# Kernel tuning notes

Measured on AMD Instinct MI355X. Metric: run time of the kernel, lower is better.

## Reference

```python
import jax, jax.numpy as jnp
import numpy as np

B, C, K, T = 8, 256, 64, 1000
NORM_EPS = 1e-12


def setup_inputs() -> dict:
    key = jax.random.key(0)
    k_x, k_codes, k_scales = jax.random.split(key, 3)
    init_val = 1.0 / (K * C) ** 0.5
    x = jax.random.normal(k_x, (B, C, T), dtype=jnp.float32)
    codes = jax.random.uniform(k_codes, (C, K), dtype=jnp.float32,
                               minval=-init_val, maxval=init_val)
    scales = jax.random.uniform(k_scales, (K,), dtype=jnp.float32,
                                minval=0.0, maxval=1.0)
    return {"x": x, "codes": codes, "scales": scales}


def l2_normalize(t, axis, eps=NORM_EPS):
    n = jnp.sqrt(jnp.sum(t * t, axis=axis, keepdims=True))
    n = jnp.maximum(n, eps)
    return t / n


def reference(x, codes, scales):
    # x: (B, C, T); codes: (C, K); scales: (K,)
    residual = x[:, :, None, :] - codes[None, :, :, None]      # (B, C, K, T)
    residual_l2sqr = jnp.sum(residual * residual, axis=1)      # (B, K, T)
    weights_tc = jax.nn.softmax(-scales[None, :, None] * residual_l2sqr, axis=1)  # softmax over codes K
    embeddings = jnp.einsum('bckt,bkt->bkc', residual, weights_tc) / x.shape[-1]  # (B, K, C)
    embeddings = l2_normalize(embeddings, axis=-1)
    return embeddings
```

## Files before the change

kernel.cpp:

```cpp
#include <hip/hip_runtime.h>
#include <stdint.h>

constexpr int Bn  = 8;
constexpr int Cn  = 256;
constexpr int Kn  = 64;
constexpr int Tn  = 1000;
constexpr int CH  = 16;
constexpr int NCH = 64;

constexpr int XT_P = 264;
constexpr int MW_P = 20;

typedef float f32x4 __attribute__((ext_vector_type(4)));
typedef __bf16 bf16x8 __attribute__((ext_vector_type(8)));

__device__ __forceinline__ unsigned short f2bf(float f) {
    unsigned u = __float_as_uint(f);
    return (unsigned short)((u + 0x7FFFu + ((u >> 16) & 1u)) >> 16);
}

union BF8 { unsigned short u[8]; bf16x8 v; };

__global__ __launch_bounds__(256) void lde_w(
    const float* __restrict__ x,
    const float* __restrict__ codes,
    const float* __restrict__ scales,
    unsigned short* __restrict__ w_g,
    float* __restrict__ Sp)
{
    __shared__ __align__(16) unsigned short xT[CH * XT_P];
    __shared__ float Mw[Kn * MW_P];
    __shared__ float xsqp[64 * 17];
    __shared__ float xsq4[64];
    __shared__ float csqs[Kn];
    __shared__ float spw[4 * 64];

    const int tid  = threadIdx.x;
    const int wave = tid >> 6;
    const int lane = tid & 63;
    const int n    = lane & 15;
    const int q    = lane >> 4;
    const int b    = blockIdx.x >> 6;
    const int ch   = blockIdx.x & 63;
    const int t0   = ch * CH;
    const float* xb = x + (size_t)b * Cn * Tn;

    {
        const int tf = tid & 3;
        float sq0 = 0.f, sq1 = 0.f, sq2 = 0.f, sq3 = 0.f;
#pragma unroll
        for (int r = 0; r < 4; ++r) {
            int c = (tid >> 2) + 64 * r;
            int t = t0 + 4 * tf;
            float4 v;
            if (t + 3 < Tn) {
                v = *(const float4*)(xb + c * Tn + t);
            } else {
                v.x = (t     < Tn) ? xb[c * Tn + t]     : 0.f;
                v.y = (t + 1 < Tn) ? xb[c * Tn + t + 1] : 0.f;
                v.z = (t + 2 < Tn) ? xb[c * Tn + t + 2] : 0.f;
                v.w = (t + 3 < Tn) ? xb[c * Tn + t + 3] : 0.f;
            }
            xT[(4 * tf + 0) * XT_P + c] = f2bf(v.x);
            xT[(4 * tf + 1) * XT_P + c] = f2bf(v.y);
            xT[(4 * tf + 2) * XT_P + c] = f2bf(v.z);
            xT[(4 * tf + 3) * XT_P + c] = f2bf(v.w);
            sq0 = fmaf(v.x, v.x, sq0);
            sq1 = fmaf(v.y, v.y, sq1);
            sq2 = fmaf(v.z, v.z, sq2);
            sq3 = fmaf(v.w, v.w, sq3);
        }
        float* xp = xsqp + (tid >> 2) * 17 + 4 * tf;
        xp[0] = sq0; xp[1] = sq1; xp[2] = sq2; xp[3] = sq3;
    }
    __syncthreads();

    if (lane < 16) {
        float a = 0.f;
#pragma unroll
        for (int i = 0; i < 16; ++i) a += xsqp[(wave * 16 + i) * 17 + lane];
        xsq4[wave * 16 + lane] = a;
    }

    {
        const int kglob = wave * 16 + n;
        const float* cod = codes + (q * 8) * Kn + kglob;
        float csq_part = 0.f;
        f32x4 acc = {0.f, 0.f, 0.f, 0.f};
#pragma unroll
        for (int c0 = 0; c0 < Cn; c0 += 32) {
            float cf[8];
#pragma unroll
            for (int j = 0; j < 8; ++j) cf[j] = cod[(size_t)(c0 + j) * Kn];
            BF8 aF;
#pragma unroll
            for (int j = 0; j < 8; ++j) {
                csq_part = fmaf(cf[j], cf[j], csq_part);
                aF.u[j] = f2bf(cf[j]);
            }
            bf16x8 bF = *(const bf16x8*)(xT + n * XT_P + c0 + q * 8);
            acc = __builtin_amdgcn_mfma_f32_16x16x32_bf16(aF.v, bF, acc, 0, 0, 0);
        }
        csq_part += __shfl_xor(csq_part, 16, 64);
        csq_part += __shfl_xor(csq_part, 32, 64);
        if (q == 0) csqs[kglob] = csq_part;
#pragma unroll
        for (int r = 0; r < 4; ++r)
            Mw[(wave * 16 + q * 4 + r) * MW_P + n] = acc[r];
    }
    __syncthreads();

    {
        const float sc = scales[lane];
        const float cq = csqs[lane];
        unsigned short wh[4];
        float sp = 0.f;
#pragma unroll
        for (int j = 0; j < 4; ++j) {
            int t = wave * 4 + j;
            float xs_t  = xsq4[t] + xsq4[16 + t] + xsq4[32 + t] + xsq4[48 + t];
            float m     = Mw[lane * MW_P + t];
            float logit = -sc * (xs_t - 2.f * m + cq);
            float mx = logit;
#pragma unroll
            for (int off = 32; off >= 1; off >>= 1)
                mx = fmaxf(mx, __shfl_xor(mx, off, 64));
            float e = __expf(logit - mx);
            float s = e;
#pragma unroll
            for (int off = 32; off >= 1; off >>= 1)
                s += __shfl_xor(s, off, 64);
            float wv = e / s;
            if (t0 + t >= Tn) wv = 0.f;
            sp += wv;
            wh[j] = f2bf(wv);
        }
        *(ushort4*)(w_g + ((size_t)(b * NCH + ch) * Kn + lane) * CH + wave * 4) =
            make_ushort4(wh[0], wh[1], wh[2], wh[3]);
        spw[wave * 64 + lane] = sp;
    }
    __syncthreads();
    if (wave == 0) {
        float s4 = spw[lane] + spw[64 + lane] + spw[128 + lane] + spw[192 + lane];
        Sp[((size_t)b * Kn + lane) * NCH + ch] = s4;
    }
}

__global__ __launch_bounds__(64) void lde_gemm(
    const float* __restrict__ x,
    const unsigned short* __restrict__ w_g,
    float* __restrict__ Ew)
{
    const int lane = threadIdx.x;
    const int n    = lane & 15;
    const int q    = lane >> 4;
    const int bid  = blockIdx.x;
    const int kt   = bid & 3;
    const int ct   = (bid >> 2) & 15;
    const int b    = bid >> 6;

    const float* xrow = x + (size_t)(b * Cn + ct * 16 + n) * Tn;
    const unsigned short* wbase =
        w_g + (size_t)b * NCH * Kn * CH + (kt * 16 + n) * CH + (q & 1) * 8;
    const int qh = q >> 1;

    f32x4 acc = {0.f, 0.f, 0.f, 0.f};
#pragma unroll 4
    for (int tc = 0; tc < 31; ++tc) {
        bf16x8 aF = *(const bf16x8*)(wbase + (size_t)(2 * tc + qh) * (Kn * CH));
        float4 v0 = *(const float4*)(xrow + tc * 32 + q * 8);
        float4 v1 = *(const float4*)(xrow + tc * 32 + q * 8 + 4);
        BF8 bF;
        bF.u[0] = f2bf(v0.x); bF.u[1] = f2bf(v0.y);
        bF.u[2] = f2bf(v0.z); bF.u[3] = f2bf(v0.w);
        bF.u[4] = f2bf(v1.x); bF.u[5] = f2bf(v1.y);
        bF.u[6] = f2bf(v1.z); bF.u[7] = f2bf(v1.w);
        acc = __builtin_amdgcn_mfma_f32_16x16x32_bf16(aF, bF.v, acc, 0, 0, 0);
    }
    {
        bf16x8 aF = *(const bf16x8*)(wbase + (size_t)(62 + qh) * (Kn * CH));
        const int tbase = 31 * 32 + q * 8;
        BF8 bF;
#pragma unroll
        for (int j = 0; j < 8; ++j) {
            int t = tbase + j;
            bF.u[j] = (t < Tn) ? f2bf(xrow[t]) : (unsigned short)0;
        }
        acc = __builtin_amdgcn_mfma_f32_16x16x32_bf16(aF, bF.v, acc, 0, 0, 0);
    }
    float* er = Ew + ((size_t)b * Kn + kt * 16 + q * 4) * Cn + ct * 16 + n;
#pragma unroll
    for (int r = 0; r < 4; ++r)
        er[(size_t)r * Cn] = acc[r];
}

__global__ __launch_bounds__(256) void lde_fin(
    const float* __restrict__ Ew,
    const float* __restrict__ Sp,
    const float* __restrict__ codes,
    float* __restrict__ out)
{
    const int b    = blockIdx.x >> 6;
    const int k    = blockIdx.x & 63;
    const int tid  = threadIdx.x;
    const int lane = tid & 63;
    const int wave = tid >> 6;

    __shared__ float red[4];
    __shared__ float Ss;

    if (wave == 0) {
        float s = Sp[((size_t)b * Kn + k) * NCH + lane];
#pragma unroll
        for (int off = 32; off >= 1; off >>= 1) s += __shfl_xor(s, off, 64);
        if (lane == 0) Ss = s;
    }
    __syncthreads();
    const float S = Ss;

    const int c = tid;
    float val = Ew[((size_t)b * Kn + k) * Cn + c];
    float e = (val - codes[c * Kn + k] * S) * (1.0f / (float)Tn);

    float qq = e * e;
#pragma unroll
    for (int off = 32; off >= 1; off >>= 1) qq += __shfl_xor(qq, off, 64);
    if (lane == 0) red[wave] = qq;
    __syncthreads();
    float nn = sqrtf(red[0] + red[1] + red[2] + red[3]);

    out[((size_t)b * Kn + k) * Cn + c] = e / fmaxf(nn, 1e-12f);
}

extern "C" void kernel_launch(void* const* d_in, const int* in_sizes, int n_in,
                              void* d_out, int out_size, void* d_ws, size_t ws_size,
                              hipStream_t stream) {
    const float* x      = (const float*)d_in[0];
    const float* codes  = (const float*)d_in[1];
    const float* scales = (const float*)d_in[2];
    float* out = (float*)d_out;

    char* ws = (char*)d_ws;
    unsigned short* w_g = (unsigned short*)ws;
    float*          Sp  = (float*)(ws + (1u << 20));
    float*          Ew  = (float*)(ws + (1u << 20) + (128u << 10));

    lde_w   <<<Bn * NCH,     256, 0, stream>>>(x, codes, scales, w_g, Sp);
    lde_gemm<<<Bn * 16 * 4,  64,  0, stream>>>(x, w_g, Ew);
    lde_fin <<<Bn * Kn,      256, 0, stream>>>(Ew, Sp, codes, out);
}
```

Baseline: 76.12 us.

## Fuse GEMM and finalize kernels, stage x as padded bf16 in workspace

The first kernel now also writes a bf16 copy of x, padded to 1024 columns with zero fill, into workspace. The separate GEMM and normalize kernels are merged into one 512-thread kernel per (batch, k-tile). Each wave computes two c-tiles from the bf16 x copy, then applies the code-weight correction and the L2 normalization in-block. This removes a kernel launch, the Ew intermediate round-trip and the per-iteration fp32-to-bf16 conversion. The cost is that the fused kernel launches only 32 blocks, which leaves most CUs idle and puts the long 32-step reduction on a few waves.

```diff
diff --git a/kernel.cpp b/kernel.cpp
--- a/kernel.cpp
+++ b/kernel.cpp
@@ -5,6 +5,7 @@
 constexpr int Cn  = 256;
 constexpr int Kn  = 64;
 constexpr int Tn  = 1000;
+constexpr int TP  = 1024;
 constexpr int CH  = 16;
 constexpr int NCH = 64;
 
@@ -25,6 +26,7 @@
     const float* __restrict__ x,
     const float* __restrict__ codes,
     const float* __restrict__ scales,
+    unsigned short* __restrict__ xbf,
     unsigned short* __restrict__ w_g,
     float* __restrict__ Sp)
 {
@@ -61,10 +63,12 @@
                 v.z = (t + 2 < Tn) ? xb[c * Tn + t + 2] : 0.f;
                 v.w = (t + 3 < Tn) ? xb[c * Tn + t + 3] : 0.f;
             }
-            xT[(4 * tf + 0) * XT_P + c] = f2bf(v.x);
-            xT[(4 * tf + 1) * XT_P + c] = f2bf(v.y);
-            xT[(4 * tf + 2) * XT_P + c] = f2bf(v.z);
-            xT[(4 * tf + 3) * XT_P + c] = f2bf(v.w);
+            ushort4 h = make_ushort4(f2bf(v.x), f2bf(v.y), f2bf(v.z), f2bf(v.w));
+            xT[(4 * tf + 0) * XT_P + c] = h.x;
+            xT[(4 * tf + 1) * XT_P + c] = h.y;
+            xT[(4 * tf + 2) * XT_P + c] = h.z;
+            xT[(4 * tf + 3) * XT_P + c] = h.w;
+            *(ushort4*)(xbf + (((size_t)(b * Cn + c)) << 10) + t0 + 4 * tf) = h;
             sq0 = fmaf(v.x, v.x, sq0);
             sq1 = fmaf(v.y, v.y, sq1);
             sq2 = fmaf(v.z, v.z, sq2);
@@ -146,90 +150,90 @@
     }
 }
 
-__global__ __launch_bounds__(64) void lde_gemm(
-    const float* __restrict__ x,
+__global__ __launch_bounds__(512) void lde_pf(
+    const unsigned short* __restrict__ xbf,
     const unsigned short* __restrict__ w_g,
-    float* __restrict__ Ew)
-{
-    const int lane = threadIdx.x;
-    const int n    = lane & 15;
-    const int q    = lane >> 4;
-    const int bid  = blockIdx.x;
-    const int kt   = bid & 3;
-    const int ct   = (bid >> 2) & 15;
-    const int b    = bid >> 6;
-
-    const float* xrow = x + (size_t)(b * Cn + ct * 16 + n) * Tn;
-    const unsigned short* wbase =
-        w_g + (size_t)b * NCH * Kn * CH + (kt * 16 + n) * CH + (q & 1) * 8;
-    const int qh = q >> 1;
-
-    f32x4 acc = {0.f, 0.f, 0.f, 0.f};
-#pragma unroll 4
-    for (int tc = 0; tc < 31; ++tc) {
-        bf16x8 aF = *(const bf16x8*)(wbase + (size_t)(2 * tc + qh) * (Kn * CH));
-        float4 v0 = *(const float4*)(xrow + tc * 32 + q * 8);
-        float4 v1 = *(const float4*)(xrow + tc * 32 + q * 8 + 4);
-        BF8 bF;
-        bF.u[0] = f2bf(v0.x); bF.u[1] = f2bf(v0.y);
-        bF.u[2] = f2bf(v0.z); bF.u[3] = f2bf(v0.w);
-        bF.u[4] = f2bf(v1.x); bF.u[5] = f2bf(v1.y);
-        bF.u[6] = f2bf(v1.z); bF.u[7] = f2bf(v1.w);
-        acc = __builtin_amdgcn_mfma_f32_16x16x32_bf16(aF, bF.v, acc, 0, 0, 0);
-    }
-    {
-        bf16x8 aF = *(const bf16x8*)(wbase + (size_t)(62 + qh) * (Kn * CH));
-        const int tbase = 31 * 32 + q * 8;
-        BF8 bF;
-#pragma unroll
-        for (int j = 0; j < 8; ++j) {
-            int t = tbase + j;
-            bF.u[j] = (t < Tn) ? f2bf(xrow[t]) : (unsigned short)0;
-        }
-        acc = __builtin_amdgcn_mfma_f32_16x16x32_bf16(aF, bF.v, acc, 0, 0, 0);
-    }
-    float* er = Ew + ((size_t)b * Kn + kt * 16 + q * 4) * Cn + ct * 16 + n;
-#pragma unroll
-    for (int r = 0; r < 4; ++r)
-        er[(size_t)r * Cn] = acc[r];
-}
-
-__global__ __launch_bounds__(256) void lde_fin(
-    const float* __restrict__ Ew,
     const float* __restrict__ Sp,
     const float* __restrict__ codes,
     float* __restrict__ out)
 {
-    const int b    = blockIdx.x >> 6;
-    const int k    = blockIdx.x & 63;
+    __shared__ float S_l[16];
+    __shared__ float normp[8 * 16];
+    __shared__ float nscale[16];
+
     const int tid  = threadIdx.x;
+    const int wave = tid >> 6;
     const int lane = tid & 63;
-    const int wave = tid >> 6;
-
-    __shared__ float red[4];
-    __shared__ float Ss;
-
-    if (wave == 0) {
-        float s = Sp[((size_t)b * Kn + k) * NCH + lane];
+    const int n    = lane & 15;
+    const int q    = lane >> 4;
+    const int b    = blockIdx.x >> 2;
+    const int kt   = blockIdx.x & 3;
+
+#pragma unroll
+    for (int j = 0; j < 2; ++j) {
+        const int kk = wave * 2 + j;
+        float s = Sp[((size_t)(b * Kn + kt * 16 + kk)) * NCH + lane];
 #pragma unroll
         for (int off = 32; off >= 1; off >>= 1) s += __shfl_xor(s, off, 64);
-        if (lane == 0) Ss = s;
-    }
-    __syncthreads();
-    const float S = Ss;
-
-    const int c = tid;
-    float val = Ew[((size_t)b * Kn + k) * Cn + c];
-    float e = (val - codes[c * Kn + k] * S) * (1.0f / (float)Tn);
-
-    float qq = e * e;
-#pragma unroll
-    for (int off = 32; off >= 1; off >>= 1) qq += __shfl_xor(qq, off, 64);
-    if (lane == 0) red[wave] = qq;
-    __syncthreads();
-    float nn = sqrtf(red[0] + red[1] + red[2] + red[3]);
-
-    out[((size_t)b * Kn + k) * Cn + c] = e / fmaxf(nn, 1e-12f);
+        if (lane == 0) S_l[kk] = s;
+    }
+
+    const int ct0 = wave;
+    const unsigned short* xr0 = xbf + (((size_t)(b * Cn + ct0 * 16 + n)) << 10) + q * 8;
+    const unsigned short* xr1 = xr0 + ((size_t)(8 * 16) << 10);
+    const unsigned short* wbase =
+        w_g + (size_t)b * NCH * Kn * CH + (kt * 16 + n) * CH + (q & 1) * 8;
+    const int qh = q >> 1;
+
+    f32x4 a0 = {0.f, 0.f, 0.f, 0.f};
+    f32x4 a1 = {0.f, 0.f, 0.f, 0.f};
+#pragma unroll 8
+    for (int tc = 0; tc < 32; ++tc) {
+        bf16x8 aF = *(const bf16x8*)(wbase + (size_t)(2 * tc + qh) * (Kn * CH));
+        bf16x8 b0 = *(const bf16x8*)(xr0 + tc * 32);
+        bf16x8 b1 = *(const bf16x8*)(xr1 + tc * 32);
+        a0 = __builtin_amdgcn_mfma_f32_16x16x32_bf16(aF, b0, a0, 0, 0, 0);
+        a1 = __builtin_amdgcn_mfma_f32_16x16x32_bf16(aF, b1, a1, 0, 0, 0);
+    }
+    __syncthreads();
+
+    const float invT = 1.0f / (float)Tn;
+    f32x4 c0v = *(const f32x4*)(codes + (ct0 * 16 + n) * Kn + kt * 16 + q * 4);
+    f32x4 c1v = *(const f32x4*)(codes + ((ct0 + 8) * 16 + n) * Kn + kt * 16 + q * 4);
+
+    float e0[4], e1[4], qq[4];
+#pragma unroll
+    for (int r = 0; r < 4; ++r) {
+        float Sr = S_l[q * 4 + r];
+        e0[r] = (a0[r] - c0v[r] * Sr) * invT;
+        e1[r] = (a1[r] - c1v[r] * Sr) * invT;
+        qq[r] = e0[r] * e0[r] + e1[r] * e1[r];
+    }
+#pragma unroll
+    for (int off = 8; off >= 1; off >>= 1) {
+#pragma unroll
+        for (int r = 0; r < 4; ++r) qq[r] += __shfl_xor(qq[r], off, 64);
+    }
+    if (n == 0) {
+#pragma unroll
+        for (int r = 0; r < 4; ++r) normp[wave * 16 + q * 4 + r] = qq[r];
+    }
+    __syncthreads();
+    if (tid < 16) {
+        float t = 0.f;
+#pragma unroll
+        for (int w = 0; w < 8; ++w) t += normp[w * 16 + tid];
+        nscale[tid] = 1.0f / fmaxf(sqrtf(t), 1e-12f);
+    }
+    __syncthreads();
+
+    float* ob = out + ((size_t)(b * Kn + kt * 16 + q * 4)) * Cn;
+#pragma unroll
+    for (int r = 0; r < 4; ++r) {
+        float ns = nscale[q * 4 + r];
+        ob[(size_t)r * Cn + ct0 * 16 + n]       = e0[r] * ns;
+        ob[(size_t)r * Cn + (ct0 + 8) * 16 + n] = e1[r] * ns;
+    }
 }
 
 extern "C" void kernel_launch(void* const* d_in, const int* in_sizes, int n_in,
@@ -241,11 +245,10 @@
     float* out = (float*)d_out;
 
     char* ws = (char*)d_ws;
-    unsigned short* w_g = (unsigned short*)ws;
-    float*          Sp  = (float*)(ws + (1u << 20));
-    float*          Ew  = (float*)(ws + (1u << 20) + (128u << 10));
-
-    lde_w   <<<Bn * NCH,     256, 0, stream>>>(x, codes, scales, w_g, Sp);
-    lde_gemm<<<Bn * 16 * 4,  64,  0, stream>>>(x, w_g, Ew);
-    lde_fin <<<Bn * Kn,      256, 0, stream>>>(Ew, Sp, codes, out);
-}
+    unsigned short* xbf = (unsigned short*)ws;
+    unsigned short* w_g = (unsigned short*)(ws + (4u << 20));
+    float*          Sp  = (float*)(ws + (5u << 20));
+
+    lde_w <<<Bn * NCH, 256, 0, stream>>>(x, codes, scales, xbf, w_g, Sp);
+    lde_pf<<<Bn * 4,   512, 0, stream>>>(xbf, w_g, Sp, codes, out);
+}
```

After: 89.88 us. +18.1%, slower.
